# Optimization experiments

Hardware: AMD Instinct MI355X
Metric: run time of the kernel (lower is better)

The kernel has to match this reference:

```python
import jax, jax.numpy as jnp
import numpy as np

H = 512
B = 32
T = 2048


def setup_inputs() -> dict:
    key = jax.random.key(0)
    ks = jax.random.split(key, 8)
    hidden = jax.random.normal(ks[0], (1, B, H), dtype=jnp.float32)
    encoder_outputs = jax.random.normal(ks[1], (T, B, H), dtype=jnp.float32)
    coverage = jax.random.uniform(ks[2], (B, T), dtype=jnp.float32)
    # nn.Linear(3H, H): weight [H, 3H], bias [H]
    W_attn = jax.random.normal(ks[3], (H, 3 * H), dtype=jnp.float32) / np.sqrt(3 * H)
    b_attn = jax.random.normal(ks[4], (H,), dtype=jnp.float32) / np.sqrt(3 * H)
    # v ~ Normal(0, 1/sqrt(H))
    v = jax.random.normal(ks[5], (H,), dtype=jnp.float32) / np.sqrt(H)
    # nn.Linear(1, H, bias=False): weight [H, 1]
    W_cov = jax.random.normal(ks[6], (H, 1), dtype=jnp.float32)
    return {"hidden": hidden, "encoder_outputs": encoder_outputs, "coverage": coverage,
            "W_attn": W_attn, "b_attn": b_attn, "v": v, "W_cov": W_cov}


def reference(hidden, encoder_outputs, coverage, W_attn, b_attn, v, W_cov):
    # hidden: [1,B,H], encoder_outputs: [T,B,H], coverage: [B,T]
    enc = jnp.transpose(encoder_outputs, (1, 0, 2))          # [B,T,H]
    b, t, h = enc.shape
    hrep = jnp.broadcast_to(hidden[0][:, None, :], (b, t, h))  # [B,T,H]
    # coverage_feature = Linear(1,H,bias=False)(coverage[...,None]) -> outer product
    cov_feat = coverage[..., None] * W_cov[:, 0]               # [B,T,H]
    x = jnp.concatenate([hrep, enc, cov_feat], axis=-1)        # [B,T,3H]
    energy = jax.nn.relu(jnp.einsum('btk,hk->bth', x, W_attn) + b_attn)  # [B,T,H]
    scores = jnp.einsum('bth,h->bt', energy, v)                # [B,T]
    attn_weights = jax.nn.softmax(scores, axis=1)              # softmax over T
    coverage_new = coverage + attn_weights                     # [B,T]
    return attn_weights[:, None, :], coverage_new
```

## Files before the change

### kernel.cpp

```cpp
#include <hip/hip_runtime.h>
#include <hip/hip_bf16.h>

typedef unsigned short u16;
typedef unsigned int u32;
typedef __attribute__((ext_vector_type(8))) short bf16x8;
typedef __attribute__((ext_vector_type(4))) float f32x4;

#define T_DIM 2048
#define B_DIM 32
#define H_DIM 512
#define M_DIM (T_DIM * B_DIM)

__device__ inline unsigned pack2(float a, float b) {
  union { __hip_bfloat162 h2; unsigned u; } c;
  c.h2 = __float22bfloat162_rn(make_float2(a, b));
  return c.u;
}

__global__ __launch_bounds__(256) void prep_kernel(
    const float* __restrict__ hidden, const float* __restrict__ W_attn,
    const float* __restrict__ b_attn, const float* __restrict__ W_cov,
    u16* __restrict__ W2bf, float* __restrict__ r, float* __restrict__ u)
{
  const int tid = blockIdx.x * 256 + threadIdx.x;
  const int pair = tid >> 2;
  const int kq = tid & 3;
  const int b = pair >> 9, h = pair & 511;

  {
    const float* hid = hidden + b * 512 + kq * 128;
    const float* w1 = W_attn + (size_t)h * 1536 + kq * 128;
    float acc = 0.f;
    #pragma unroll 8
    for (int k = 0; k < 128; k += 4) {
      float4 x = *(const float4*)(hid + k);
      float4 w = *(const float4*)(w1 + k);
      acc += x.x * w.x + x.y * w.y + x.z * w.z + x.w * w.w;
    }
    acc += __shfl_xor(acc, 1);
    acc += __shfl_xor(acc, 2);
    if (kq == 0) r[pair] = acc + b_attn[h];
  }

  {
    int j0 = tid * 4;
    int hh = j0 >> 9, kk = j0 & 511;
    float4 w = *(const float4*)(W_attn + (size_t)hh * 1536 + 512 + kk);
    uint2 p;
    p.x = pack2(w.x, w.y);
    p.y = pack2(w.z, w.w);
    int f = hh >> 4, c = hh & 15;
    int ks = kk >> 5, quad = (kk >> 3) & 3, e = kk & 7;
    *(uint2*)(W2bf + (size_t)((f * 16 + ks) * 64 + quad * 16 + c) * 8 + e) = p;
  }

  if (tid < 2048) {
    int h3 = tid >> 2;
    const float* w3 = W_attn + (size_t)h3 * 1536 + 1024 + kq * 128;
    const float* wc = W_cov + kq * 128;
    float su = 0.f;
    #pragma unroll 8
    for (int k = 0; k < 128; k += 4) {
      float4 a = *(const float4*)(w3 + k);
      float4 c = *(const float4*)(wc + k);
      su += a.x * c.x + a.y * c.y + a.z * c.z + a.w * c.w;
    }
    su += __shfl_xor(su, 1);
    su += __shfl_xor(su, 2);
    if (kq == 0) u[h3] = su;
  }
}

__global__ __launch_bounds__(512, 4) void gemm_score(
    const float* __restrict__ enc, const u16* __restrict__ W2bf,
    const float* __restrict__ r, const float* __restrict__ u,
    const float* __restrict__ vv, const float* __restrict__ cov,
    float* __restrict__ part)
{
  const int m0 = blockIdx.x * 64;
  const int tid = threadIdx.x;
  const int lane = tid & 63;
  const int w = tid >> 6;
  const int quad = lane >> 4, col = lane & 15;

  __shared__ u16 As[64 * 512];

  float4 buf[16];
  {
    const float* gbase = enc + (size_t)m0 * 512 + lane * 8;
    #pragma unroll
    for (int it = 0; it < 8; ++it) {
      const float* ga = gbase + (size_t)(it * 8 + w) * 512;
      buf[it * 2]     = *(const float4*)ga;
      buf[it * 2 + 1] = *(const float4*)(ga + 4);
    }
  }
  #pragma unroll
  for (int it = 0; it < 8; ++it) {
    int row = it * 8 + w;
    uint4 p;
    p.x = pack2(buf[it * 2].x,     buf[it * 2].y);
    p.y = pack2(buf[it * 2].z,     buf[it * 2].w);
    p.z = pack2(buf[it * 2 + 1].x, buf[it * 2 + 1].y);
    p.w = pack2(buf[it * 2 + 1].z, buf[it * 2 + 1].w);
    *(uint4*)&As[row * 512 + (lane ^ (row & 7)) * 8] = p;
  }
  __syncthreads();

  f32x4 acc[4][4] = {};
  const u16* bbase = W2bf + (size_t)w * 32768 + lane * 8;

  bf16x8 bcur[4], bnxt[4];
  #pragma unroll
  for (int j = 0; j < 4; ++j)
    bcur[j] = *(const bf16x8*)(bbase + j * 8192);

  #pragma unroll
  for (int ks = 0; ks < 16; ++ks) {
    if (ks < 15) {
      #pragma unroll
      for (int j = 0; j < 4; ++j)
        bnxt[j] = *(const bf16x8*)(bbase + j * 8192 + (ks + 1) * 512);
    }
    #pragma unroll
    for (int i = 0; i < 4; ++i) {
      int row = i * 16 + col;
      bf16x8 af = *(const bf16x8*)&As[row * 512 + ((ks * 4 + quad) ^ (col & 7)) * 8];
      #pragma unroll
      for (int j = 0; j < 4; ++j)
        acc[i][j] = __builtin_amdgcn_mfma_f32_16x16x32_bf16(af, bcur[j], acc[i][j], 0, 0, 0);
    }
    #pragma unroll
    for (int j = 0; j < 4; ++j) bcur[j] = bnxt[j];
  }

  float uj[4], vj[4];
  #pragma unroll
  for (int j = 0; j < 4; ++j) {
    int gh = w * 64 + j * 16 + col;
    uj[j] = u[gh];
    vj[j] = vv[gh];
  }
  #pragma unroll
  for (int pr = 0; pr < 2; ++pr) {
    #pragma unroll
    for (int reg = 0; reg < 4; ++reg) {
      int b = pr * 16 + quad * 4 + reg;
      const float* rb = r + b * 512;
      float rbj[4];
      #pragma unroll
      for (int j = 0; j < 4; ++j) rbj[j] = rb[w * 64 + j * 16 + col];
      #pragma unroll
      for (int isub = 0; isub < 2; ++isub) {
        int i = pr + isub * 2;
        int t = (m0 >> 5) + isub;
        float cv = cov[b * 2048 + t];
        float s = 0.f;
        #pragma unroll
        for (int j = 0; j < 4; ++j) {
          float e = acc[i][j][reg] + rbj[j] + cv * uj[j];
          e = fmaxf(e, 0.f);
          s += e * vj[j];
        }
        s += __shfl_xor(s, 1);
        s += __shfl_xor(s, 2);
        s += __shfl_xor(s, 4);
        s += __shfl_xor(s, 8);
        if (col == 0) part[(size_t)(w * 32 + b) * 2048 + t] = s;
      }
    }
  }
}

__global__ __launch_bounds__(256) void softmax_kernel(
    const float* __restrict__ part, const float* __restrict__ cov, float* __restrict__ out)
{
  const int b = blockIdx.x;
  const int tid = threadIdx.x;
  const int lane = tid & 63, wid = tid >> 6;
  __shared__ float red[4];
  float loc[8];
  float lmax = -3.4e38f;
  #pragma unroll
  for (int i = 0; i < 8; ++i) {
    int t = tid + i * 256;
    float s = 0.f;
    #pragma unroll
    for (int p = 0; p < 8; ++p) s += part[(size_t)(p * 32 + b) * 2048 + t];
    loc[i] = s;
    lmax = fmaxf(lmax, s);
  }
  #pragma unroll
  for (int o = 32; o; o >>= 1) lmax = fmaxf(lmax, __shfl_xor(lmax, o));
  if (lane == 0) red[wid] = lmax;
  __syncthreads();
  float bmax = fmaxf(fmaxf(red[0], red[1]), fmaxf(red[2], red[3]));
  __syncthreads();
  float lsum = 0.f;
  #pragma unroll
  for (int i = 0; i < 8; ++i) { loc[i] = __expf(loc[i] - bmax); lsum += loc[i]; }
  #pragma unroll
  for (int o = 32; o; o >>= 1) lsum += __shfl_xor(lsum, o);
  if (lane == 0) red[wid] = lsum;
  __syncthreads();
  float inv = 1.0f / (red[0] + red[1] + red[2] + red[3]);
  #pragma unroll
  for (int i = 0; i < 8; ++i) {
    int t = tid + i * 256;
    float a = loc[i] * inv;
    out[b * 2048 + t] = a;
    out[65536 + b * 2048 + t] = cov[b * 2048 + t] + a;
  }
}

extern "C" void kernel_launch(void* const* d_in, const int* in_sizes, int n_in,
                              void* d_out, int out_size, void* d_ws, size_t ws_size,
                              hipStream_t stream) {
  const float* hidden = (const float*)d_in[0];
  const float* enc    = (const float*)d_in[1];
  const float* cov    = (const float*)d_in[2];
  const float* W_attn = (const float*)d_in[3];
  const float* b_attn = (const float*)d_in[4];
  const float* vv     = (const float*)d_in[5];
  const float* W_cov  = (const float*)d_in[6];
  float* out = (float*)d_out;

  u16* W2bf = (u16*)d_ws;
  float* r  = (float*)((char*)d_ws + 512 * 1024);
  float* u  = r + 32 * 512;
  float* part = u + 512;

  hipLaunchKernelGGL(prep_kernel, dim3(256), dim3(256), 0, stream,
                     hidden, W_attn, b_attn, W_cov, W2bf, r, u);
  hipLaunchKernelGGL(gemm_score, dim3(1024), dim3(512), 0, stream,
                     enc, W2bf, r, u, vv, cov, part);
  hipLaunchKernelGGL(softmax_kernel, dim3(32), dim3(256), 0, stream,
                     part, cov, out);
}
```

Baseline: 270.2 us.

## Load encoder tile directly into LDS as fp32 and halve the GEMM M-tile

The encoder tile is now staged with global_load_lds straight into shared memory as fp32, replacing the register round trip and bf16 packing before the store. Conversion to bf16 moves into the MFMA inner loop, so each A fragment is packed on the fly. The block tile shrinks from 64 to 32 rows (one timestep), which doubles the grid and halves the accumulators. The cost is repeated W2 fragment loads per block, because there are twice as many blocks, plus extra conversion ALU work inside the loop.

```diff
diff --git a/kernel.cpp b/kernel.cpp
--- a/kernel.cpp
+++ b/kernel.cpp
@@ -15,6 +15,12 @@
   union { __hip_bfloat162 h2; unsigned u; } c;
   c.h2 = __float22bfloat162_rn(make_float2(a, b));
   return c.u;
+}
+
+__device__ __forceinline__ void gld16(const void* g, void* s) {
+  __builtin_amdgcn_global_load_lds(
+      (const __attribute__((address_space(1))) void*)g,
+      (__attribute__((address_space(3))) void*)s, 16, 0, 0);
 }
 
 __global__ __launch_bounds__(256) void prep_kernel(
@@ -77,43 +83,35 @@
     const float* __restrict__ vv, const float* __restrict__ cov,
     float* __restrict__ part)
 {
-  const int m0 = blockIdx.x * 64;
+  const int t = blockIdx.x;
+  const int m0 = t * 32;
   const int tid = threadIdx.x;
   const int lane = tid & 63;
   const int w = tid >> 6;
   const int quad = lane >> 4, col = lane & 15;
 
-  __shared__ u16 As[64 * 512];
-
-  float4 buf[16];
-  {
-    const float* gbase = enc + (size_t)m0 * 512 + lane * 8;
-    #pragma unroll
-    for (int it = 0; it < 8; ++it) {
-      const float* ga = gbase + (size_t)(it * 8 + w) * 512;
-      buf[it * 2]     = *(const float4*)ga;
-      buf[it * 2 + 1] = *(const float4*)(ga + 4);
-    }
-  }
-  #pragma unroll
-  for (int it = 0; it < 8; ++it) {
-    int row = it * 8 + w;
-    uint4 p;
-    p.x = pack2(buf[it * 2].x,     buf[it * 2].y);
-    p.y = pack2(buf[it * 2].z,     buf[it * 2].w);
-    p.z = pack2(buf[it * 2 + 1].x, buf[it * 2 + 1].y);
-    p.w = pack2(buf[it * 2 + 1].z, buf[it * 2 + 1].w);
-    *(uint4*)&As[row * 512 + (lane ^ (row & 7)) * 8] = p;
-  }
-  __syncthreads();
-
-  f32x4 acc[4][4] = {};
+  __shared__ float As[32 * 512];
+
+  #pragma unroll
+  for (int q = 0; q < 8; ++q) {
+    int n = w * 8 + q;
+    int rr = n >> 1, hh = n & 1;
+    int gsrc = hh * 64 + (lane ^ (rr & 7));
+    gld16(enc + (size_t)(m0 + rr) * 512 + gsrc * 4, (void*)(As + n * 256));
+  }
+  __syncthreads();
+
+  f32x4 acc[2][4] = {};
   const u16* bbase = W2bf + (size_t)w * 32768 + lane * 8;
 
   bf16x8 bcur[4], bnxt[4];
   #pragma unroll
   for (int j = 0; j < 4; ++j)
     bcur[j] = *(const bf16x8*)(bbase + j * 8192);
+
+  const int o0 = (((quad * 2)    ) ^ (col & 7)) * 4;
+  const int o1 = (((quad * 2) + 1) ^ (col & 7)) * 4;
+  const float* arow0 = As + col * 512;
 
   #pragma unroll
   for (int ks = 0; ks < 16; ++ks) {
@@ -123,12 +121,18 @@
         bnxt[j] = *(const bf16x8*)(bbase + j * 8192 + (ks + 1) * 512);
     }
     #pragma unroll
-    for (int i = 0; i < 4; ++i) {
-      int row = i * 16 + col;
-      bf16x8 af = *(const bf16x8*)&As[row * 512 + ((ks * 4 + quad) ^ (col & 7)) * 8];
+    for (int i = 0; i < 2; ++i) {
+      const float* ap = arow0 + i * 8192 + ks * 32;
+      float4 f0 = *(const float4*)(ap + o0);
+      float4 f1 = *(const float4*)(ap + o1);
+      union { bf16x8 v; u32 uu[4]; } af;
+      af.uu[0] = pack2(f0.x, f0.y);
+      af.uu[1] = pack2(f0.z, f0.w);
+      af.uu[2] = pack2(f1.x, f1.y);
+      af.uu[3] = pack2(f1.z, f1.w);
       #pragma unroll
       for (int j = 0; j < 4; ++j)
-        acc[i][j] = __builtin_amdgcn_mfma_f32_16x16x32_bf16(af, bcur[j], acc[i][j], 0, 0, 0);
+        acc[i][j] = __builtin_amdgcn_mfma_f32_16x16x32_bf16(af.v, bcur[j], acc[i][j], 0, 0, 0);
     }
     #pragma unroll
     for (int j = 0; j < 4; ++j) bcur[j] = bnxt[j];
@@ -142,32 +146,24 @@
     vj[j] = vv[gh];
   }
   #pragma unroll
-  for (int pr = 0; pr < 2; ++pr) {
+  for (int i = 0; i < 2; ++i) {
     #pragma unroll
     for (int reg = 0; reg < 4; ++reg) {
-      int b = pr * 16 + quad * 4 + reg;
-      const float* rb = r + b * 512;
-      float rbj[4];
+      int b = i * 16 + quad * 4 + reg;
+      float cv = cov[b * 2048 + t];
+      float s = 0.f;
       #pragma unroll
-      for (int j = 0; j < 4; ++j) rbj[j] = rb[w * 64 + j * 16 + col];
-      #pragma unroll
-      for (int isub = 0; isub < 2; ++isub) {
-        int i = pr + isub * 2;
-        int t = (m0 >> 5) + isub;
-        float cv = cov[b * 2048 + t];
-        float s = 0.f;
-        #pragma unroll
-        for (int j = 0; j < 4; ++j) {
-          float e = acc[i][j][reg] + rbj[j] + cv * uj[j];
-          e = fmaxf(e, 0.f);
-          s += e * vj[j];
-        }
-        s += __shfl_xor(s, 1);
-        s += __shfl_xor(s, 2);
-        s += __shfl_xor(s, 4);
-        s += __shfl_xor(s, 8);
-        if (col == 0) part[(size_t)(w * 32 + b) * 2048 + t] = s;
+      for (int j = 0; j < 4; ++j) {
+        float rv = r[b * 512 + w * 64 + j * 16 + col];
+        float e = acc[i][j][reg] + rv + cv * uj[j];
+        e = fmaxf(e, 0.f);
+        s += e * vj[j];
       }
+      s += __shfl_xor(s, 1);
+      s += __shfl_xor(s, 2);
+      s += __shfl_xor(s, 4);
+      s += __shfl_xor(s, 8);
+      if (col == 0) part[(size_t)(w * 32 + b) * 2048 + t] = s;
     }
   }
 }
@@ -232,7 +228,7 @@
 
   hipLaunchKernelGGL(prep_kernel, dim3(256), dim3(256), 0, stream,
                      hidden, W_attn, b_attn, W_cov, W2bf, r, u);
-  hipLaunchKernelGGL(gemm_score, dim3(1024), dim3(512), 0, stream,
+  hipLaunchKernelGGL(gemm_score, dim3(2048), dim3(512), 0, stream,
                      enc, W2bf, r, u, vv, cov, part);
   hipLaunchKernelGGL(softmax_kernel, dim3(32), dim3(256), 0, stream,
                      part, cov, out);
```

Result: slower. 280.6 us (+3.8%).
